# Optimization experiments

Hardware: AMD Instinct MI355X
Metric: run time of the kernel (lower is better)

## Reference

```python
import jax, jax.numpy as jnp
import numpy as np

D_NODE = 100
D_HID = 300
EPS = 1e-5


def _gru_step_h0(x, W_ih, b_ih, b_hh):
    # Single torch-GRU step with h0 = 0 (seq len 1), so W_hh @ h0 vanishes
    # and only the hidden biases b_hh survive.
    gi = x @ W_ih.T + b_ih                      # [..., 3*H]
    H = D_HID
    r = jax.nn.sigmoid(gi[..., 0:H] + b_hh[0:H])
    z = jax.nn.sigmoid(gi[..., H:2 * H] + b_hh[H:2 * H])
    n = jnp.tanh(gi[..., 2 * H:3 * H] + r * b_hh[2 * H:3 * H])
    return (1.0 - z) * n                        # h' = (1-z)*n + z*0


def setup_inputs() -> dict:
    key = jax.random.key(0)
    ks = jax.random.split(key, 20)
    B, T, Lq, N = 128, 512, 256, 256
    s = 0.02
    inp = {
        "nodes": jax.random.normal(ks[0], (B * N, D_NODE), jnp.float32),
        "context_rep": jax.random.normal(ks[1], (B, Lq, D_HID), jnp.float32),
        "dia_triples": jax.random.randint(ks[2], (B, T, 3), 0, N, jnp.int64 if jax.config.jax_enable_x64 else jnp.int32),
        "node_number": N,
        # mean_trans: Linear(100, 300)
        "W_mean": s * jax.random.normal(ks[3], (D_HID, D_NODE), jnp.float32),
        "b_mean": jnp.zeros((D_HID,), jnp.float32),
        # bidirectional GRU(300 -> 300); h0=0 so W_hh drops out, keep biases
        "W_ih_f": s * jax.random.normal(ks[4], (3 * D_HID, D_HID), jnp.float32),
        "b_ih_f": s * jax.random.normal(ks[5], (3 * D_HID,), jnp.float32),
        "b_hh_f": s * jax.random.normal(ks[6], (3 * D_HID,), jnp.float32),
        "W_ih_b": s * jax.random.normal(ks[7], (3 * D_HID, D_HID), jnp.float32),
        "b_ih_b": s * jax.random.normal(ks[8], (3 * D_HID,), jnp.float32),
        "b_hh_b": s * jax.random.normal(ks[9], (3 * D_HID,), jnp.float32),
        # output_trans: Linear(600, 300) + tanh
        "W_out": s * jax.random.normal(ks[10], (D_HID, 2 * D_HID), jnp.float32),
        "b_out": jnp.zeros((D_HID,), jnp.float32),
        # trans_node_to_decoder_dim: Linear(100, 300)
        "W_node": s * jax.random.normal(ks[11], (D_HID, D_NODE), jnp.float32),
        "b_node": jnp.zeros((D_HID,), jnp.float32),
        # layernorm(300)
        "gamma": jnp.ones((D_HID,), jnp.float32),
        "beta": jnp.zeros((D_HID,), jnp.float32),
    }
    return inp


def reference(nodes, context_rep, dia_triples, node_number,
              W_mean, b_mean, W_ih_f, b_ih_f, b_hh_f,
              W_ih_b, b_ih_b, b_hh_b, W_out, b_out,
              W_node, b_node, gamma, beta):
    B = context_rep.shape[0]
    N = node_number
    T = dia_triples.shape[1]
    nodes3 = nodes.reshape(B, N, D_NODE)                        # per-dialogue node slices

    # gather head/tail nodes of each triple, mean-aggregate
    head = jnp.broadcast_to(dia_triples[:, :, 0][:, :, None], (B, T, D_NODE))
    tail = jnp.broadcast_to(dia_triples[:, :, -1][:, :, None], (B, T, D_NODE))
    gh = jnp.take_along_axis(nodes3, head, axis=1)              # [B,T,100]
    gt = jnp.take_along_axis(nodes3, tail, axis=1)
    tri_mean = 0.5 * (gh + gt)

    x = tri_mean @ W_mean.T + b_mean                            # [B,T,300] GRU inputs (len-1 paths)

    # bidirectional GRU, one step each direction from h0=0
    h_f = _gru_step_h0(x, W_ih_f, b_ih_f, b_hh_f)
    h_b = _gru_step_h0(x, W_ih_b, b_ih_b, b_hh_b)
    hidden = jnp.concatenate([h_f, h_b], axis=-1)               # [B,T,600]

    hid_ = jnp.tanh(hidden @ W_out.T + b_out)                   # [B,T,300]

    # attention: alpha = softmax(query @ hidden^T, -1).sum(0)
    scores = jnp.einsum("bld,btd->blt", context_rep, hid_)
    alpha = jax.nn.softmax(scores, axis=-1).sum(axis=1)         # [B,T]
    rep = jnp.einsum("bt,btd->bd", alpha, hid_)                 # [B,300]

    mu = rep.mean(axis=-1, keepdims=True)
    var = rep.var(axis=-1, keepdims=True)
    path_feature = (rep - mu) * jax.lax.rsqrt(var + EPS) * gamma + beta
    # dropout is identity in eval mode

    node_feature = nodes3 @ W_node.T + b_node                   # [B,N,300]
    node_mask = jnp.zeros((B, 1, N), dtype=bool)                # equal lengths -> no padding
    return path_feature, node_feature, node_mask
```

## Files before the change

### kernel.cpp

```cpp
#include <hip/hip_runtime.h>
#include <math.h>

#define D_NODE 100
#define D_HID  300
static const int TSEQ = 512, LQn = 256, NNODE = 256;

typedef unsigned int u32;
typedef unsigned short u16;
typedef __attribute__((ext_vector_type(8))) short bf16x8;
typedef __attribute__((ext_vector_type(4))) float f32x4;

__device__ __forceinline__ float bf2f(u16 v){ return __uint_as_float(((u32)v) << 16); }
__device__ __forceinline__ u16 f2bf(float f){
    u32 u = __float_as_uint(f);
    return (u16)((u + 0x7fffu + ((u >> 16) & 1u)) >> 16);
}
__device__ __forceinline__ u32 pack_bf(float lo, float hi){
    return ((u32)f2bf(lo)) | (((u32)f2bf(hi)) << 16);
}
__device__ __forceinline__ void gload_lds16(const void* g, void* l){
    __builtin_amdgcn_global_load_lds(
        (const __attribute__((address_space(1))) u32*)g,
        (__attribute__((address_space(3))) u32*)l, 16, 0, 0);
}
__device__ __forceinline__ float fsig(float x){
    return __builtin_amdgcn_rcpf(1.f + __expf(-x));
}
__device__ __forceinline__ float ftanh(float x){
    return 1.f - 2.f*__builtin_amdgcn_rcpf(1.f + __expf(2.f*x));
}

__global__ __launch_bounds__(128)
void k0_prep(const float* __restrict__ Wm, const float* __restrict__ bm,
             const float* __restrict__ Wihf, const float* __restrict__ bihf, const float* __restrict__ bhhf,
             const float* __restrict__ Wihb, const float* __restrict__ bihb, const float* __restrict__ bhhb,
             u16* __restrict__ W4bf, float* __restrict__ bc, float* __restrict__ bhhn)
{
    int j = blockIdx.x, g = blockIdx.y, dir = blockIdx.z;
    int tid = threadIdx.x;
    u16* wout = W4bf + ((size_t)((dir*3+g)*320 + j))*128;
    if (j >= D_HID) {
        wout[tid] = 0;
        if (tid == 0) { bc[(dir*3+g)*320 + j] = 0.f; if (g==2) bhhn[dir*320+j] = 0.f; }
        return;
    }
    const float* Wih = dir ? Wihb : Wihf;
    const float* bih = dir ? bihb : bihf;
    const float* bhh = dir ? bhhb : bhhf;
    const float* wrow = Wih + (size_t)(g*D_HID + j)*D_HID;
    int k = tid;
    float s = 0.f;
    if (k < D_NODE)
        for (int q = 0; q < D_HID; ++q)
            s = fmaf(wrow[q], Wm[q*D_NODE + k], s);
    wout[k] = f2bf(k < D_NODE ? s : 0.f);

    __shared__ float red[128];
    float p = 0.f;
    for (int q = tid; q < D_HID; q += 128) p = fmaf(bm[q], wrow[q], p);
    red[tid] = p;
    __syncthreads();
    for (int off = 64; off > 0; off >>= 1) {
        if (tid < off) red[tid] += red[tid + off];
        __syncthreads();
    }
    if (tid == 0) {
        float base = bih[g*D_HID + j] + red[0];
        if (g < 2) base += bhh[g*D_HID + j];
        bc[(dir*3+g)*320 + j] = base;
        if (g == 2) bhhn[dir*320 + j] = bhh[2*D_HID + j];
    }
}

__global__ __launch_bounds__(256)
void kW(const float* __restrict__ Wout, const float* __restrict__ Wnode,
        u16* __restrict__ Woutbf, u16* __restrict__ Wnbf)
{
    int idx = blockIdx.x*256 + threadIdx.x;
    if (idx < 320*640) {
        int j = idx / 640, k = idx % 640;
        float v = 0.f;
        if (j < D_HID) {
            if (k < D_HID)                 v = Wout[(size_t)j*600 + k];
            else if (k >= 320 && k < 620)  v = Wout[(size_t)j*600 + (k - 20)];
        }
        Woutbf[idx] = f2bf(v);
    } else {
        int i2 = idx - 320*640;
        if (i2 < 320*128) {
            int j = i2 >> 7, k = i2 & 127;
            float v = (j < D_HID && k < D_NODE) ? Wnode[(size_t)j*D_NODE + k] : 0.f;
            Wnbf[i2] = f2bf(v);
        }
    }
}

__global__ __launch_bounds__(256)
void kA(const float* __restrict__ nodes, const int* __restrict__ trip,
        u32* __restrict__ Abf, u32* __restrict__ Nbf)
{
    int wid  = (blockIdx.x*256 + threadIdx.x) >> 6;
    int nw   = (gridDim.x*256) >> 6;
    int lane = threadIdx.x & 63;
    for (int r = wid; r < 98304; r += nw) {
        if (r < 65536) {
            int b = r >> 9;
            int h  = trip[(size_t)r*3];
            int t2 = trip[(size_t)r*3 + 2];
            const float* nh = nodes + ((size_t)b*NNODE + h)*D_NODE;
            const float* nt = nodes + ((size_t)b*NNODE + t2)*D_NODE;
            u32 v = 0;
            if (lane < 50) {
                float2 a = *(const float2*)(nh + lane*2);
                float2 c = *(const float2*)(nt + lane*2);
                v = pack_bf(0.5f*(a.x + c.x), 0.5f*(a.y + c.y));
            }
            Abf[(size_t)r*64 + lane] = v;
        } else {
            int q = r - 65536;
            u32 v = 0;
            if (lane < 50) {
                float2 a = *(const float2*)(nodes + (size_t)q*D_NODE + lane*2);
                v = pack_bf(a.x, a.y);
            }
            Nbf[(size_t)q*64 + lane] = v;
        }
    }
}

__global__ __launch_bounds__(256)
void kC(const float* __restrict__ ctx, u32* __restrict__ Cbf)
{
    int idx = blockIdx.x*256 + threadIdx.x;
    int r = idx / 40, cp = idx % 40;
    int col = cp*8;
    uint4 v = {0,0,0,0};
    if (col < D_HID) {
        const float* base = ctx + (size_t)r*D_HID + col;
        float4 f0 = *(const float4*)base;
        v.x = pack_bf(f0.x, f0.y); v.y = pack_bf(f0.z, f0.w);
        if (col + 8 <= D_HID) {
            float4 f1 = *(const float4*)(base + 4);
            v.z = pack_bf(f1.x, f1.y); v.w = pack_bf(f1.z, f1.w);
        }
    }
    *(uint4*)(Cbf + (size_t)r*160 + cp*4) = v;
}

__global__ __launch_bounds__(256, 2)
void k1_gru(const u16* __restrict__ Abf, const u16* __restrict__ W4bf,
            const float* __restrict__ bc, const float* __restrict__ bhhn,
            u16* __restrict__ H)
{
    __shared__ __attribute__((aligned(16))) char smem[16384];
    int tid = threadIdx.x;
    int lane = tid & 63, w = tid >> 6;
    int l15 = lane & 15, lq = lane >> 4;
    int m0 = blockIdx.x * 64;
    const int dir = blockIdx.y;

    #pragma unroll
    for (int ks = 0; ks < 4; ++ks) {
        const u16* g = Abf + ((size_t)(m0 + w*16 + l15))*128 + ks*32 + lq*8;
        gload_lds16(g, smem + (size_t)((w*4 + ks)*64)*16);
    }
    __syncthreads();

    bf16x8 af[4][4];
    #pragma unroll
    for (int ms = 0; ms < 4; ++ms)
        #pragma unroll
        for (int ks = 0; ks < 4; ++ks)
            af[ms][ks] = *(const bf16x8*)(smem + (size_t)(((ms*4+ks)*64 + lane))*16);

    const u16* Wb = W4bf + (size_t)dir*3*320*128;
    #pragma unroll
    for (int jg = 0; jg < 5; ++jg) {
        const int j0w = jg*64 + w*16;
        const int j = j0w + l15;

        bf16x8 bfr[3][4];
        #pragma unroll
        for (int g = 0; g < 3; ++g)
            #pragma unroll
            for (int ks = 0; ks < 4; ++ks)
                bfr[g][ks] = *(const bf16x8*)(Wb + ((size_t)(g*320 + j0w + l15))*128 + ks*32 + lq*8);

        f32x4 acc[4][3];
        #pragma unroll
        for (int ms = 0; ms < 4; ++ms)
            #pragma unroll
            for (int g = 0; g < 3; ++g)
                acc[ms][g] = (f32x4){0.f,0.f,0.f,0.f};

        #pragma unroll
        for (int ms = 0; ms < 4; ++ms)
            #pragma unroll
            for (int ks = 0; ks < 4; ++ks) {
                acc[ms][0] = __builtin_amdgcn_mfma_f32_16x16x32_bf16(af[ms][ks], bfr[0][ks], acc[ms][0], 0,0,0);
                acc[ms][1] = __builtin_amdgcn_mfma_f32_16x16x32_bf16(af[ms][ks], bfr[1][ks], acc[ms][1], 0,0,0);
                acc[ms][2] = __builtin_amdgcn_mfma_f32_16x16x32_bf16(af[ms][ks], bfr[2][ks], acc[ms][2], 0,0,0);
            }

        float bcr = bc[(dir*3+0)*320 + j];
        float bcz = bc[(dir*3+1)*320 + j];
        float bcn = bc[(dir*3+2)*320 + j];
        float bn2 = bhhn[dir*320 + j];
        bool ok = (j < D_HID);
        #pragma unroll
        for (int ms = 0; ms < 4; ++ms)
            #pragma unroll
            for (int i = 0; i < 4; ++i) {
                float r = fsig(acc[ms][0][i] + bcr);
                float z = fsig(acc[ms][1][i] + bcz);
                float n = ftanh(acc[ms][2][i] + bcn + r*bn2);
                float h = (1.f - z)*n;
                H[(size_t)(m0 + ms*16 + lq*4 + i)*640 + dir*320 + j] = ok ? f2bf(h) : (u16)0;
            }
    }
}

__global__ __launch_bounds__(256, 2)
void k2_out(const u16* __restrict__ H, const u16* __restrict__ Woutbf,
            const float* __restrict__ bout, u16* __restrict__ Hid)
{
    __shared__ __attribute__((aligned(16))) char smem[8192];
    int tid = threadIdx.x;
    int lane = tid & 63, w = tid >> 6;
    int l15 = lane & 15, lq = lane >> 4;
    int m0 = blockIdx.x * 64;

    f32x4 acc[4][5];
    #pragma unroll
    for (int ms = 0; ms < 4; ++ms)
        #pragma unroll
        for (int jj = 0; jj < 5; ++jj)
            acc[ms][jj] = (f32x4){0.f,0.f,0.f,0.f};

    for (int c = 0; c < 10; ++c) {
        #pragma unroll
        for (int r = 0; r < 2; ++r) {
            int p = w*2 + r, pm = p >> 1, pk = p & 1;
            gload_lds16(H + ((size_t)(m0 + pm*16 + l15))*640 + c*64 + pk*32 + lq*8,
                        smem + (size_t)(p*64)*16);
        }
        __syncthreads();
        #pragma unroll
        for (int pk = 0; pk < 2; ++pk) {
            bf16x8 bb[5];
            #pragma unroll
            for (int jj = 0; jj < 5; ++jj)
                bb[jj] = *(const bf16x8*)(Woutbf + ((size_t)(w*80 + jj*16 + l15))*640 + c*64 + pk*32 + lq*8);
            #pragma unroll
            for (int ms = 0; ms < 4; ++ms) {
                bf16x8 a = *(const bf16x8*)(smem + (size_t)(((ms*2+pk)*64 + lane))*16);
                #pragma unroll
                for (int jj = 0; jj < 5; ++jj)
                    acc[ms][jj] = __builtin_amdgcn_mfma_f32_16x16x32_bf16(a, bb[jj], acc[ms][jj], 0,0,0);
            }
        }
        __syncthreads();
    }

    #pragma unroll
    for (int jj = 0; jj < 5; ++jj) {
        int j = w*80 + jj*16 + l15;
        bool real = (j < D_HID);
        float bo = real ? bout[j] : 0.f;
        #pragma unroll
        for (int ms = 0; ms < 4; ++ms)
            #pragma unroll
            for (int i = 0; i < 4; ++i) {
                u16 v = real ? f2bf(ftanh(acc[ms][jj][i] + bo)) : (u16)0;
                Hid[(size_t)(m0 + ms*16 + lq*4 + i)*320 + j] = v;
            }
    }
}

__global__ __launch_bounds__(256, 2)
void k3_attn(const u16* __restrict__ Cbf, const u16* __restrict__ Hid,
             float* __restrict__ alphap)
{
    __shared__ char smemA[4096];
    __shared__ char smemB[32768];
    __shared__ float rmax[64*4], rsum[64*4];
    int tid = threadIdx.x;
    int lane = tid & 63, w = tid >> 6;
    int l15 = lane & 15, lq = lane >> 4;
    int id = blockIdx.x;
    int xcd = id & 7, s = id >> 3;
    int bq = s >> 2, mblk = s & 3;
    int b = bq*8 + xcd;
    const u16* Ab = Cbf + ((size_t)b*LQn + mblk*64)*320;
    const u16* Bb = Hid + ((size_t)b*TSEQ)*320;

    f32x4 acc[4][8];
    #pragma unroll
    for (int ms = 0; ms < 4; ++ms)
        #pragma unroll
        for (int g = 0; g < 8; ++g)
            acc[ms][g] = (f32x4){0,0,0,0};

    for (int ks = 0; ks < 10; ++ks) {
        gload_lds16(Ab + ((size_t)(w*16 + l15))*320 + ks*32 + lq*8,
                    smemA + (size_t)(w*64)*16);
        #pragma unroll
        for (int i = 0; i < 8; ++i) {
            int nt = w*8 + i;
            gload_lds16(Bb + ((size_t)(nt*16 + l15))*320 + ks*32 + lq*8,
                        smemB + (size_t)(nt*64)*16);
        }
        __syncthreads();
        bf16x8 afr[4];
        #pragma unroll
        for (int ms = 0; ms < 4; ++ms)
            afr[ms] = *(const bf16x8*)(smemA + (size_t)((ms*64 + lane))*16);
        #pragma unroll
        for (int i = 0; i < 8; ++i) {
            bf16x8 bfr = *(const bf16x8*)(smemB + (size_t)(((w*8+i)*64 + lane))*16);
            #pragma unroll
            for (int ms = 0; ms < 4; ++ms)
                acc[ms][i] = __builtin_amdgcn_mfma_f32_16x16x32_bf16(afr[ms], bfr, acc[ms][i], 0,0,0);
        }
        __syncthreads();
    }

    #pragma unroll
    for (int ms = 0; ms < 4; ++ms)
        #pragma unroll
        for (int i = 0; i < 4; ++i) {
            float m = acc[ms][0][i];
            #pragma unroll
            for (int g = 1; g < 8; ++g) m = fmaxf(m, acc[ms][g][i]);
            m = fmaxf(m, __shfl_xor(m, 1));
            m = fmaxf(m, __shfl_xor(m, 2));
            m = fmaxf(m, __shfl_xor(m, 4));
            m = fmaxf(m, __shfl_xor(m, 8));
            if (l15 == 0) rmax[(ms*16 + lq*4 + i)*4 + w] = m;
        }
    __syncthreads();
    float mfin[4][4];
    #pragma unroll
    for (int ms = 0; ms < 4; ++ms)
        #pragma unroll
        for (int i = 0; i < 4; ++i) {
            float4 mv = *(const float4*)&rmax[(ms*16 + lq*4 + i)*4];
            mfin[ms][i] = fmaxf(fmaxf(mv.x, mv.y), fmaxf(mv.z, mv.w));
        }
    #pragma unroll
    for (int ms = 0; ms < 4; ++ms)
        #pragma unroll
        for (int i = 0; i < 4; ++i) {
            float s2 = 0.f;
            #pragma unroll
            for (int g = 0; g < 8; ++g) {
                float e = __expf(acc[ms][g][i] - mfin[ms][i]);
                acc[ms][g][i] = e;
                s2 += e;
            }
            s2 += __shfl_xor(s2, 1);
            s2 += __shfl_xor(s2, 2);
            s2 += __shfl_xor(s2, 4);
            s2 += __shfl_xor(s2, 8);
            if (l15 == 0) rsum[(ms*16 + lq*4 + i)*4 + w] = s2;
        }
    __syncthreads();
    float inv[4][4];
    #pragma unroll
    for (int ms = 0; ms < 4; ++ms)
        #pragma unroll
        for (int i = 0; i < 4; ++i) {
            float4 sv = *(const float4*)&rsum[(ms*16 + lq*4 + i)*4];
            inv[ms][i] = __builtin_amdgcn_rcpf(sv.x + sv.y + sv.z + sv.w);
        }
    float* ap = alphap + ((size_t)b*4 + mblk)*TSEQ;
    #pragma unroll
    for (int g = 0; g < 8; ++g) {
        float c = 0.f;
        #pragma unroll
        for (int ms = 0; ms < 4; ++ms)
            #pragma unroll
            for (int i = 0; i < 4; ++i)
                c = fmaf(acc[ms][g][i], inv[ms][i], c);
        c += __shfl_xor(c, 16);
        c += __shfl_xor(c, 32);
        if (lq == 0) ap[w*128 + g*16 + l15] = c;
    }
}

__global__ __launch_bounds__(640)
void k4_rep(const float* __restrict__ alphap, const u16* __restrict__ Hid,
            const float* __restrict__ gamma, const float* __restrict__ beta,
            float* __restrict__ outP)
{
    __shared__ float al[512];
    __shared__ float part[320];
    __shared__ float rs[10], rss[10];
    int tid = threadIdx.x, b = blockIdx.x;
    const float* ap = alphap + (size_t)b*4*TSEQ;
    for (int i = tid; i < 512; i += 640)
        al[i] = ap[i] + ap[512 + i] + ap[1024 + i] + ap[1536 + i];
    __syncthreads();
    int half = (tid >= 320) ? 1 : 0;
    int c = tid - half*320;
    float acc = 0.f;
    if (c < D_HID) {
        const u16* hp = Hid + (size_t)b*TSEQ*320 + (size_t)half*256*320 + c;
        #pragma unroll 8
        for (int t = 0; t < 256; ++t)
            acc = fmaf(al[half*256 + t], bf2f(hp[(size_t)t*320]), acc);
    }
    if (half) part[c] = acc;
    __syncthreads();
    float tot = 0.f;
    if (!half) tot = acc + part[c];
    float v = (!half && c < D_HID) ? tot : 0.f;
    float s = v, q = v*v;
    #pragma unroll
    for (int off = 32; off > 0; off >>= 1) { s += __shfl_xor(s, off, 64); q += __shfl_xor(q, off, 64); }
    if ((tid & 63) == 0) { rs[tid >> 6] = s; rss[tid >> 6] = q; }
    __syncthreads();
    float S = rs[0]+rs[1]+rs[2]+rs[3]+rs[4]+rs[5]+rs[6]+rs[7]+rs[8]+rs[9];
    float Q = rss[0]+rss[1]+rss[2]+rss[3]+rss[4]+rss[5]+rss[6]+rss[7]+rss[8]+rss[9];
    float mu = S * (1.f/300.f);
    float var = Q * (1.f/300.f) - mu*mu;
    if (!half && c < D_HID)
        outP[(size_t)b*D_HID + c] = (tot - mu) * rsqrtf(var + 1e-5f) * gamma[c] + beta[c];
}

__global__ __launch_bounds__(256)
void k5_node(const u16* __restrict__ Nbf, const u16* __restrict__ Wnbf,
             const float* __restrict__ bn, float* __restrict__ outN)
{
    __shared__ char smem[16384];
    int tid = threadIdx.x;
    int lane = tid & 63, w = tid >> 6;
    int l15 = lane & 15, lq = lane >> 4;
    int m0 = blockIdx.x * 64;
    int j0w = blockIdx.y*64 + w*16;

    bf16x8 bw[4];
    #pragma unroll
    for (int ks = 0; ks < 4; ++ks)
        bw[ks] = *(const bf16x8*)(Wnbf + ((size_t)(j0w + l15))*128 + ks*32 + lq*8);

    #pragma unroll
    for (int ks = 0; ks < 4; ++ks) {
        const u16* g = Nbf + ((size_t)(m0 + w*16 + l15))*128 + ks*32 + lq*8;
        gload_lds16(g, smem + (size_t)((w*4 + ks)*64)*16);
    }
    __syncthreads();

    f32x4 acc[4];
    #pragma unroll
    for (int ms = 0; ms < 4; ++ms) acc[ms] = (f32x4){0,0,0,0};
    #pragma unroll
    for (int ms = 0; ms < 4; ++ms)
        #pragma unroll
        for (int ks = 0; ks < 4; ++ks) {
            bf16x8 a = *(const bf16x8*)(smem + (size_t)(((ms*4+ks)*64 + lane))*16);
            acc[ms] = __builtin_amdgcn_mfma_f32_16x16x32_bf16(a, bw[ks], acc[ms], 0,0,0);
        }

    int j = j0w + l15;
    if (j < D_HID) {
        float bo = bn[j];
        #pragma unroll
        for (int ms = 0; ms < 4; ++ms)
            #pragma unroll
            for (int i = 0; i < 4; ++i)
                outN[(size_t)(m0 + ms*16 + lq*4 + i)*D_HID + j] = acc[ms][i] + bo;
    }
}

extern "C" void kernel_launch(void* const* d_in, const int* in_sizes, int n_in,
                              void* d_out, int out_size, void* d_ws, size_t ws_size,
                              hipStream_t stream) {
    const float* nodes  = (const float*)d_in[0];
    const float* ctx    = (const float*)d_in[1];
    const int*   trip   = (const int*)d_in[2];
    const float* Wm     = (const float*)d_in[4];
    const float* bm     = (const float*)d_in[5];
    const float* Wihf   = (const float*)d_in[6];
    const float* bihf   = (const float*)d_in[7];
    const float* bhhf   = (const float*)d_in[8];
    const float* Wihb   = (const float*)d_in[9];
    const float* bihb   = (const float*)d_in[10];
    const float* bhhb   = (const float*)d_in[11];
    const float* Wout   = (const float*)d_in[12];
    const float* bout   = (const float*)d_in[13];
    const float* Wnode  = (const float*)d_in[14];
    const float* bnode  = (const float*)d_in[15];
    const float* gamma  = (const float*)d_in[16];
    const float* beta   = (const float*)d_in[17];
    float* out = (float*)d_out;

    char* ws = (char*)d_ws;
    u16*   W4bf   = (u16*)(ws);
    u16*   Woutbf = (u16*)(ws + 491520);
    u16*   Wnbf   = (u16*)(ws + 901120);
    float* bc     = (float*)(ws + 983040);
    float* bhhn   = (float*)(ws + 990720);
    u32*   Abf    = (u32*)(ws + 1048576);
    u32*   Nbf    = (u32*)(ws + 17825792ull);
    u16*   Hhalf  = (u16*)(ws + 26214400ull);
    u32*   Cbf    = (u32*)(ws + 26214400ull);
    u16*   Hid    = (u16*)(ws + 68157440ull);
    float* alphap = (float*)(ws + 110100480ull);

    k0_prep<<<dim3(320,3,2), 128, 0, stream>>>(Wm,bm,Wihf,bihf,bhhf,Wihb,bihb,bhhb,W4bf,bc,bhhn);
    kW     <<<960,  256, 0, stream>>>(Wout,Wnode,Woutbf,Wnbf);
    kA     <<<1024, 256, 0, stream>>>(nodes,trip,Abf,Nbf);

    for (int h = 0; h < 2; ++h) {
        const u16* Ah   = (const u16*)Abf + (size_t)h*32768*128;
        u16*       Hidh = Hid + (size_t)h*32768*320;
        k1_gru<<<dim3(512,2), 256, 0, stream>>>(Ah, W4bf, bc, bhhn, Hhalf);
        k2_out<<<512, 256, 0, stream>>>(Hhalf, Woutbf, bout, Hidh);
    }

    k5_node<<<dim3(512,5), 256, 0, stream>>>((const u16*)Nbf,Wnbf,bnode,out + 38400);
    kC     <<<5120, 256, 0, stream>>>(ctx, Cbf);
    k3_attn<<<512,         256, 0, stream>>>((const u16*)Cbf, Hid, alphap);
    k4_rep <<<128,         640, 0, stream>>>(alphap,Hid,gamma,beta,out);
    hipMemsetAsync(out + 38400 + 9830400, 0, 32768*sizeof(float), stream);
}
```

Baseline: 403.6 us.

## Merge GRU directions per block, drop LDS staging, split rep accumulators

k1_gru now handles both GRU directions within one block, looping over 10 stages instead of launching a second grid dimension. Its A fragments are loaded straight from global memory rather than staged through LDS, so each A tile is read once for both directions and the barrier goes away. k2_out also drops its LDS staging and barriers, reads A fragments directly from global over 20 K-steps, and relaxes launch bounds. k4_rep splits its dot-product accumulator in two to add ILP. The risks are fewer blocks in k1, uncoalesced direct global fragment loads, and higher register pressure in k2.

Result: slower. 420.8 us (+4.3%).

```diff
diff --git a/kernel.cpp b/kernel.cpp
--- a/kernel.cpp
+++ b/kernel.cpp
@@ -152,32 +152,25 @@
             const float* __restrict__ bc, const float* __restrict__ bhhn,
             u16* __restrict__ H)
 {
-    __shared__ __attribute__((aligned(16))) char smem[16384];
     int tid = threadIdx.x;
     int lane = tid & 63, w = tid >> 6;
     int l15 = lane & 15, lq = lane >> 4;
     int m0 = blockIdx.x * 64;
-    const int dir = blockIdx.y;
-
-    #pragma unroll
-    for (int ks = 0; ks < 4; ++ks) {
-        const u16* g = Abf + ((size_t)(m0 + w*16 + l15))*128 + ks*32 + lq*8;
-        gload_lds16(g, smem + (size_t)((w*4 + ks)*64)*16);
-    }
-    __syncthreads();
 
     bf16x8 af[4][4];
     #pragma unroll
     for (int ms = 0; ms < 4; ++ms)
         #pragma unroll
         for (int ks = 0; ks < 4; ++ks)
-            af[ms][ks] = *(const bf16x8*)(smem + (size_t)(((ms*4+ks)*64 + lane))*16);
-
-    const u16* Wb = W4bf + (size_t)dir*3*320*128;
-    #pragma unroll
-    for (int jg = 0; jg < 5; ++jg) {
+            af[ms][ks] = *(const bf16x8*)(Abf + ((size_t)(m0 + ms*16 + l15))*128 + ks*32 + lq*8);
+
+    #pragma unroll
+    for (int st = 0; st < 10; ++st) {
+        const int dir = (st < 5) ? 0 : 1;
+        const int jg  = (st < 5) ? st : st - 5;
         const int j0w = jg*64 + w*16;
         const int j = j0w + l15;
+        const u16* Wb = W4bf + (size_t)dir*3*320*128;
 
         bf16x8 bfr[3][4];
         #pragma unroll
@@ -220,11 +213,10 @@
     }
 }
 
-__global__ __launch_bounds__(256, 2)
+__global__ __launch_bounds__(256)
 void k2_out(const u16* __restrict__ H, const u16* __restrict__ Woutbf,
             const float* __restrict__ bout, u16* __restrict__ Hid)
 {
-    __shared__ __attribute__((aligned(16))) char smem[8192];
     int tid = threadIdx.x;
     int lane = tid & 63, w = tid >> 6;
     int l15 = lane & 15, lq = lane >> 4;
@@ -237,29 +229,20 @@
         for (int jj = 0; jj < 5; ++jj)
             acc[ms][jj] = (f32x4){0.f,0.f,0.f,0.f};
 
-    for (int c = 0; c < 10; ++c) {
-        #pragma unroll
-        for (int r = 0; r < 2; ++r) {
-            int p = w*2 + r, pm = p >> 1, pk = p & 1;
-            gload_lds16(H + ((size_t)(m0 + pm*16 + l15))*640 + c*64 + pk*32 + lq*8,
-                        smem + (size_t)(p*64)*16);
-        }
-        __syncthreads();
-        #pragma unroll
-        for (int pk = 0; pk < 2; ++pk) {
-            bf16x8 bb[5];
+    for (int kk = 0; kk < 20; ++kk) {
+        bf16x8 bb[5];
+        #pragma unroll
+        for (int jj = 0; jj < 5; ++jj)
+            bb[jj] = *(const bf16x8*)(Woutbf + ((size_t)(w*80 + jj*16 + l15))*640 + kk*32 + lq*8);
+        bf16x8 a[4];
+        #pragma unroll
+        for (int ms = 0; ms < 4; ++ms)
+            a[ms] = *(const bf16x8*)(H + ((size_t)(m0 + ms*16 + l15))*640 + kk*32 + lq*8);
+        #pragma unroll
+        for (int ms = 0; ms < 4; ++ms)
             #pragma unroll
             for (int jj = 0; jj < 5; ++jj)
-                bb[jj] = *(const bf16x8*)(Woutbf + ((size_t)(w*80 + jj*16 + l15))*640 + c*64 + pk*32 + lq*8);
-            #pragma unroll
-            for (int ms = 0; ms < 4; ++ms) {
-                bf16x8 a = *(const bf16x8*)(smem + (size_t)(((ms*2+pk)*64 + lane))*16);
-                #pragma unroll
-                for (int jj = 0; jj < 5; ++jj)
-                    acc[ms][jj] = __builtin_amdgcn_mfma_f32_16x16x32_bf16(a, bb[jj], acc[ms][jj], 0,0,0);
-            }
-        }
-        __syncthreads();
+                acc[ms][jj] = __builtin_amdgcn_mfma_f32_16x16x32_bf16(a[ms], bb[jj], acc[ms][jj], 0,0,0);
     }
 
     #pragma unroll
@@ -406,9 +389,13 @@
     float acc = 0.f;
     if (c < D_HID) {
         const u16* hp = Hid + (size_t)b*TSEQ*320 + (size_t)half*256*320 + c;
-        #pragma unroll 8
-        for (int t = 0; t < 256; ++t)
-            acc = fmaf(al[half*256 + t], bf2f(hp[(size_t)t*320]), acc);
+        float a0 = 0.f, a1 = 0.f;
+        #pragma unroll 4
+        for (int t = 0; t < 256; t += 2) {
+            a0 = fmaf(al[half*256 + t],     bf2f(hp[(size_t)t*320]),       a0);
+            a1 = fmaf(al[half*256 + t + 1], bf2f(hp[(size_t)(t+1)*320]),   a1);
+        }
+        acc = a0 + a1;
     }
     if (half) part[c] = acc;
     __syncthreads();
@@ -515,7 +502,7 @@
     for (int h = 0; h < 2; ++h) {
         const u16* Ah   = (const u16*)Abf + (size_t)h*32768*128;
         u16*       Hidh = Hid + (size_t)h*32768*320;
-        k1_gru<<<dim3(512,2), 256, 0, stream>>>(Ah, W4bf, bc, bhhn, Hhalf);
+        k1_gru<<<512, 256, 0, stream>>>(Ah, W4bf, bc, bhhn, Hhalf);
         k2_out<<<512, 256, 0, stream>>>(Hhalf, Woutbf, bout, Hidh);
     }
 
```
